# Kernel tuning notes

Hardware: AMD Instinct MI355X
Metric: run time of the kernel (lower is better)

Reference implementation:

```python
import jax, jax.numpy as jnp
import numpy as np

N = 50000      # nodes
E = 800000     # edges (before self-loops)
HEADS = 4
IN = 128
HID = 96
DH = HID // HEADS  # 24 per-head channels
G = 64         # graphs in batch
OUT = 3


def setup_inputs() -> dict:
    key = jax.random.key(0)
    ks = jax.random.split(key, 16)
    def w(k, shape, fan):
        return (jax.random.normal(k, shape, jnp.float32) * (fan ** -0.5)).astype(jnp.float32)
    x = jax.random.normal(ks[0], (N, IN), jnp.float32)
    edge_index = jax.random.randint(ks[1], (2, E), 0, N, dtype=jnp.int32)
    batch = jnp.sort(jax.random.randint(ks[2], (N,), 0, G, dtype=jnp.int32))
    return {
        'x': x, 'edge_index': edge_index, 'batch': batch, 'num_graphs': G,
        'W1': w(ks[3], (IN, HID), IN),
        'att_src1': w(ks[4], (HEADS, DH), DH),
        'att_dst1': w(ks[5], (HEADS, DH), DH),
        'b1': jnp.zeros((HID,), jnp.float32),
        'W2': w(ks[6], (HID, HID), HID),
        'att_src2': w(ks[7], (HEADS, DH), DH),
        'att_dst2': w(ks[8], (HEADS, DH), DH),
        'b2': jnp.zeros((HID,), jnp.float32),
        'g_w1': w(ks[9], (HID, HID // 2), HID),
        'g_b1': jnp.zeros((HID // 2,), jnp.float32),
        'g_w2': w(ks[10], (HID // 2, 1), HID // 2),
        'g_b2': jnp.zeros((1,), jnp.float32),
        'f_w1': w(ks[11], (HID, HID), HID),
        'f_b1': jnp.zeros((HID,), jnp.float32),
        'f_w2': w(ks[12], (HID, OUT), HID),
        'f_b2': jnp.zeros((OUT,), jnp.float32),
    }


def _gat_layer(x, src, dst, W, a_src, a_dst, b, n):
    # x: [n, F]; src/dst: [E'] (self-loops included). PyG GATConv math.
    h = (x @ W).reshape(n, HEADS, DH)                 # [n, H, d]
    alpha_s = jnp.sum(h * a_src[None], axis=-1)       # [n, H]
    alpha_d = jnp.sum(h * a_dst[None], axis=-1)       # [n, H]
    e = jax.nn.leaky_relu(alpha_s[src] + alpha_d[dst], 0.2)  # [E', H]
    # segment softmax over incoming edges of each dst node
    m = jax.ops.segment_max(e, dst, num_segments=n)   # [n, H]
    ex = jnp.exp(e - m[dst])
    denom = jax.ops.segment_sum(ex, dst, num_segments=n)
    alpha = ex / (denom[dst] + 1e-16)                 # [E', H]
    msg = h[src] * alpha[:, :, None]                  # [E', H, d]
    out = jax.ops.segment_sum(msg, dst, num_segments=n)
    return out.reshape(n, HEADS * DH) + b


def reference(x, edge_index, batch, num_graphs, W1, att_src1, att_dst1, b1,
              W2, att_src2, att_dst2, b2, g_w1, g_b1, g_w2, g_b2,
              f_w1, f_b1, f_w2, f_b2):
    n = x.shape[0]
    loops = jnp.arange(n, dtype=edge_index.dtype)
    src = jnp.concatenate([edge_index[0], loops])     # add self-loops (PyG default)
    dst = jnp.concatenate([edge_index[1], loops])
    h = jax.nn.elu(_gat_layer(x, src, dst, W1, att_src1, att_dst1, b1, n))
    h = jax.nn.elu(_gat_layer(h, src, dst, W2, att_src2, att_dst2, b2, n))
    # GlobalAttention pool: gate_nn -> softmax over batch segments -> weighted sum
    gate = (jax.nn.relu(h @ g_w1 + g_b1) @ g_w2 + g_b2)[:, 0]   # [n]
    gm = jax.ops.segment_max(gate, batch, num_segments=num_graphs)
    gm = jnp.where(jnp.isfinite(gm), gm, 0.0)
    ge = jnp.exp(gate - gm[batch])
    gden = jax.ops.segment_sum(ge, batch, num_segments=num_graphs)
    wgt = ge / (gden[batch] + 1e-16)                  # [n]
    pooled = jax.ops.segment_sum(h * wgt[:, None], batch, num_segments=num_graphs)  # [G, HID]
    return jax.nn.relu(pooled @ f_w1 + f_b1) @ f_w2 + f_b2   # [G, 3]
```

## Files before the change

### kernel.cpp

```cpp
#include <hip/hip_runtime.h>
#include <cmath>


__global__ void init_deg_kernel(int* __restrict__ deg, int n) {
    int i = blockIdx.x * blockDim.x + threadIdx.x;
    if (i < n) deg[i] = 1;
}

__global__ void hist_kernel(const int* __restrict__ dst, int* __restrict__ deg, int E) {
    int e = blockIdx.x * blockDim.x + threadIdx.x;
    if (e < E) atomicAdd(&deg[dst[e]], 1);
}

__global__ void scan_bsum_kernel(const int* __restrict__ deg, int* __restrict__ bsum, int n) {
    __shared__ int s[256];
    int t = threadIdx.x;
    int base = blockIdx.x * 1024;
    int sum = 0;
#pragma unroll
    for (int j = 0; j < 4; j++) {
        int i = base + j * 256 + t;
        if (i < n) sum += deg[i];
    }
    s[t] = sum;
    __syncthreads();
    for (int off = 128; off; off >>= 1) {
        if (t < off) s[t] += s[t + off];
        __syncthreads();
    }
    if (t == 0) bsum[blockIdx.x] = s[0];
}

__global__ void scan_bsum_scan_kernel(int* __restrict__ bsum, int nb,
                                      int* __restrict__ rowptr, int n) {
    __shared__ int s[256];
    int t = threadIdx.x;
    int v = (t < nb) ? bsum[t] : 0;
    s[t] = v;
    __syncthreads();
    for (int off = 1; off < 256; off <<= 1) {
        int x = (t >= off) ? s[t - off] : 0;
        __syncthreads();
        s[t] += x;
        __syncthreads();
    }
    if (t < nb) bsum[t] = s[t] - v;
    if (t == 255) rowptr[n] = s[255];
}

__global__ void scan_local_kernel(const int* __restrict__ deg, const int* __restrict__ bsum,
                                  int* __restrict__ rowptr, int* __restrict__ pos, int n) {
    __shared__ int s[256];
    int t = threadIdx.x;
    int base = blockIdx.x * 1024;
    int d[4];
    int sum = 0;
#pragma unroll
    for (int j = 0; j < 4; j++) {
        int i = base + t * 4 + j;
        d[j] = (i < n) ? deg[i] : 0;
        sum += d[j];
    }
    s[t] = sum;
    __syncthreads();
    for (int off = 1; off < 256; off <<= 1) {
        int x = (t >= off) ? s[t - off] : 0;
        __syncthreads();
        s[t] += x;
        __syncthreads();
    }
    int run = bsum[blockIdx.x] + s[t] - sum;
#pragma unroll
    for (int j = 0; j < 4; j++) {
        int i = base + t * 4 + j;
        if (i < n) { rowptr[i] = run; pos[i] = run; }
        run += d[j];
    }
}

__global__ void fill_kernel(const int* __restrict__ src, const int* __restrict__ dst,
                            int* __restrict__ pos, int* __restrict__ col, int E, int N) {
    int i = blockIdx.x * blockDim.x + threadIdx.x;
    if (i < E) {
        int p = atomicAdd(&pos[dst[i]], 1);
        col[p] = src[i];
    } else if (i < E + N) {
        int n = i - E;
        int p = atomicAdd(&pos[n], 1);
        col[p] = n;
    }
}

template<int K, int NCOL, int TN, int MODE>
__global__ __launch_bounds__(256)
void tiled_gemm_kernel(const float* __restrict__ X, const float* __restrict__ W,
                       const float* __restrict__ v1, const float* __restrict__ v2,
                       const float* __restrict__ v3,
                       float* __restrict__ H, float* __restrict__ AS, float* __restrict__ AD,
                       int n_nodes) {
    const int t = threadIdx.x;
    const int tx = t & 15, ty = t >> 4;
    const int c0 = tx * TN;
    const int m0 = ty * 4;
    const int node0 = blockIdx.x * 64;

    __shared__ float As[16][68];
    __shared__ float Bs[16][NCOL];

    float acc[4][TN];
#pragma unroll
    for (int i = 0; i < 4; i++)
#pragma unroll
        for (int j = 0; j < TN; j++) acc[i][j] = 0.f;

    const int am = t >> 2, akq = t & 3;

    for (int kb = 0; kb < K; kb += 16) {
        float4 av = make_float4(0.f, 0.f, 0.f, 0.f);
        int anode = node0 + am;
        if (anode < n_nodes)
            av = *reinterpret_cast<const float4*>(X + (size_t)anode * K + kb + akq * 4);
        As[akq * 4 + 0][am] = av.x;
        As[akq * 4 + 1][am] = av.y;
        As[akq * 4 + 2][am] = av.z;
        As[akq * 4 + 3][am] = av.w;
        {
            const float4* wsrc = reinterpret_cast<const float4*>(W + (size_t)kb * NCOL);
            float4* bdst = reinterpret_cast<float4*>(&Bs[0][0]);
            for (int i = t; i < 16 * NCOL / 4; i += 256) bdst[i] = wsrc[i];
        }
        __syncthreads();
#pragma unroll
        for (int k = 0; k < 16; k++) {
            float4 a4 = *reinterpret_cast<const float4*>(&As[k][m0]);
            float a[4] = {a4.x, a4.y, a4.z, a4.w};
            float b[TN];
            if constexpr ((TN & 1) == 0) {
#pragma unroll
                for (int j = 0; j < TN / 2; j++) {
                    float2 b2 = *reinterpret_cast<const float2*>(&Bs[k][c0 + 2 * j]);
                    b[2 * j] = b2.x; b[2 * j + 1] = b2.y;
                }
            } else {
#pragma unroll
                for (int j = 0; j < TN; j++) b[j] = Bs[k][c0 + j];
            }
#pragma unroll
            for (int i = 0; i < 4; i++)
#pragma unroll
                for (int j = 0; j < TN; j++)
                    acc[i][j] = fmaf(a[i], b[j], acc[i][j]);
        }
        __syncthreads();
    }

    if constexpr (MODE == 0) {
        __shared__ float s_as[64][16];
        __shared__ float s_ad[64][16];
#pragma unroll
        for (int i = 0; i < 4; i++) {
            int node = node0 + m0 + i;
            float asp = 0.f, adp = 0.f;
#pragma unroll
            for (int j = 0; j < TN; j++) {
                asp = fmaf(acc[i][j], v1[c0 + j], asp);
                adp = fmaf(acc[i][j], v2[c0 + j], adp);
            }
            s_as[m0 + i][tx] = asp;
            s_ad[m0 + i][tx] = adp;
            if (node < n_nodes) {
#pragma unroll
                for (int j = 0; j < TN / 2; j++) {
                    float2 o;
                    o.x = acc[i][2 * j]; o.y = acc[i][2 * j + 1];
                    *reinterpret_cast<float2*>(H + (size_t)node * NCOL + c0 + 2 * j) = o;
                }
            }
        }
        __syncthreads();
        int m = t >> 2, head = t & 3;
        int node = node0 + m;
        if (node < n_nodes) {
            float s1 = s_as[m][head * 4 + 0] + s_as[m][head * 4 + 1]
                     + s_as[m][head * 4 + 2] + s_as[m][head * 4 + 3];
            float s2 = s_ad[m][head * 4 + 0] + s_ad[m][head * 4 + 1]
                     + s_ad[m][head * 4 + 2] + s_ad[m][head * 4 + 3];
            AS[(size_t)node * 4 + head] = s1;
            AD[(size_t)node * 4 + head] = s2;
        }
    } else {
        __shared__ float s_g[64][16];
#pragma unroll
        for (int i = 0; i < 4; i++) {
            float p = 0.f;
#pragma unroll
            for (int j = 0; j < TN; j++) {
                float a = acc[i][j] + v1[c0 + j];
                a = fmaxf(a, 0.f);
                p = fmaf(a, v2[c0 + j], p);
            }
            s_g[m0 + i][tx] = p;
        }
        __syncthreads();
        if (t < 64) {
            int node = node0 + t;
            if (node < n_nodes) {
                float s = 0.f;
#pragma unroll
                for (int j = 0; j < 16; j++) s += s_g[t][j];
                H[node] = s + v3[0];
            }
        }
    }
}

__global__ __launch_bounds__(256)
void gat_agg_wave_kernel(const float* __restrict__ H, const float* __restrict__ AS,
                         const float* __restrict__ AD, const int* __restrict__ rowptr,
                         const int* __restrict__ col, const float* __restrict__ bias,
                         float* __restrict__ OUT, int n_nodes) {
    int wid = threadIdx.x >> 6;
    int lane = threadIdx.x & 63;
    int n = blockIdx.x * 4 + wid;
    if (n >= n_nodes) return;
    int beg = rowptr[n];
    int deg = rowptr[n + 1] - beg;

    int h = lane & 3;
    int slot = lane >> 2;
    float ad_n = AD[(size_t)n * 4 + h];

    float mymax = -INFINITY;
    for (int i = slot; i < deg; i += 16) {
        int s = col[beg + i];
        float v = AS[(size_t)s * 4 + h] + ad_n;
        v = v > 0.f ? v : 0.2f * v;
        mymax = fmaxf(mymax, v);
    }
#pragma unroll
    for (int m = 4; m <= 32; m <<= 1)
        mymax = fmaxf(mymax, __shfl_xor(mymax, m, 64));
    float m_h = mymax;

    int c = lane;
    bool cown = c < 48;
    int head_c = cown ? (c / 12) : 0;
    const float2* __restrict__ Hc = reinterpret_cast<const float2*>(H) + c;

    float denom_part = 0.f;
    float2 acc0 = make_float2(0.f, 0.f), acc1 = make_float2(0.f, 0.f);
    float2 acc2 = make_float2(0.f, 0.f), acc3 = make_float2(0.f, 0.f);

    for (int base = 0; base < deg; base += 16) {
        int ce = base + slot;
        int s_e = 0;
        float ex = 0.f;
        if (ce < deg) {
            s_e = col[beg + ce];
            float v = AS[(size_t)s_e * 4 + h] + ad_n;
            v = v > 0.f ? v : 0.2f * v;
            ex = __expf(v - m_h);
        }
        denom_part += ex;
        int cnt = min(16, deg - base);

        int sbv[16];
        float wv[16];
#pragma unroll
        for (int i = 0; i < 16; i++) {
            sbv[i] = __shfl(s_e, i * 4, 64);
            wv[i]  = __shfl(ex,  i * 4 + head_c, 64);
        }

#pragma unroll
        for (int g = 0; g < 16; g += 4) {
            if (g < cnt && cown) {
                float2 v0 = Hc[(size_t)sbv[g + 0] * 48];
                float2 v1 = Hc[(size_t)sbv[g + 1] * 48];
                float2 v2 = Hc[(size_t)sbv[g + 2] * 48];
                float2 v3 = Hc[(size_t)sbv[g + 3] * 48];
                acc0.x = fmaf(v0.x, wv[g + 0], acc0.x);
                acc0.y = fmaf(v0.y, wv[g + 0], acc0.y);
                acc1.x = fmaf(v1.x, wv[g + 1], acc1.x);
                acc1.y = fmaf(v1.y, wv[g + 1], acc1.y);
                acc2.x = fmaf(v2.x, wv[g + 2], acc2.x);
                acc2.y = fmaf(v2.y, wv[g + 2], acc2.y);
                acc3.x = fmaf(v3.x, wv[g + 3], acc3.x);
                acc3.y = fmaf(v3.y, wv[g + 3], acc3.y);
            }
        }
    }

#pragma unroll
    for (int m = 4; m <= 32; m <<= 1)
        denom_part += __shfl_xor(denom_part, m, 64);
    float den = __shfl(denom_part, head_c, 64);

    if (cown) {
        float2 acc;
        acc.x = (acc0.x + acc1.x) + (acc2.x + acc3.x);
        acc.y = (acc0.y + acc1.y) + (acc2.y + acc3.y);
        float2 b2 = reinterpret_cast<const float2*>(bias)[c];
        float inv = 1.f / (den + 1e-16f);
        float ox = acc.x * inv + b2.x;
        float oy = acc.y * inv + b2.y;
        ox = ox > 0.f ? ox : (__expf(ox) - 1.f);
        oy = oy > 0.f ? oy : (__expf(oy) - 1.f);
        reinterpret_cast<float2*>(OUT)[(size_t)n * 48 + c] = make_float2(ox, oy);
    }
}

__device__ __forceinline__ int lower_bound_dev(const int* __restrict__ arr, int n, int key) {
    int lo = 0, hi = n;
    while (lo < hi) {
        int mid = (lo + hi) >> 1;
        if (arr[mid] < key) lo = mid + 1; else hi = mid;
    }
    return lo;
}

__global__ void gate_stats_kernel(const float* __restrict__ gate, const int* __restrict__ batch,
                                  int n_nodes, float* __restrict__ gm_out,
                                  float* __restrict__ inv_gden_out, float* __restrict__ pooled) {
    int g = blockIdx.x, t = threadIdx.x;
    if (t < 96) pooled[(size_t)g * 96 + t] = 0.f;
    __shared__ int sb, se;
    __shared__ float sred[256];
    if (t == 0) {
        sb = lower_bound_dev(batch, n_nodes, g);
        se = lower_bound_dev(batch, n_nodes, g + 1);
    }
    __syncthreads();
    int beg = sb, end = se;

    float mx = -INFINITY;
    for (int i = beg + t; i < end; i += 256) mx = fmaxf(mx, gate[i]);
    sred[t] = mx;
    __syncthreads();
    for (int off = 128; off; off >>= 1) {
        if (t < off) sred[t] = fmaxf(sred[t], sred[t + off]);
        __syncthreads();
    }
    float gm = sred[0];
    if (!isfinite(gm)) gm = 0.f;
    __syncthreads();

    float sm = 0.f;
    for (int i = beg + t; i < end; i += 256) sm += __expf(gate[i] - gm);
    sred[t] = sm;
    __syncthreads();
    for (int off = 128; off; off >>= 1) {
        if (t < off) sred[t] += sred[t + off];
        __syncthreads();
    }
    if (t == 0) {
        gm_out[g] = gm;
        inv_gden_out[g] = 1.f / (sred[0] + 1e-16f);
    }
}

__global__ __launch_bounds__(384)
void pool_accum_kernel(const float* __restrict__ H2, const float* __restrict__ gate,
                       const int* __restrict__ batch, const float* __restrict__ gm,
                       const float* __restrict__ inv_gden, int n_nodes,
                       float* __restrict__ pooled) {
    const int NPB = 256;
    int t = threadIdx.x;
    int group = t / 96;
    int c = t - group * 96;
    if (group >= 4) return;
    int nbeg = blockIdx.x * NPB;
    int nend = min(nbeg + NPB, n_nodes);

    float acc = 0.f;
    int curg = -1;
    for (int i = nbeg + group; i < nend; i += 4) {
        int g = batch[i];
        if (g != curg) {
            if (curg >= 0) atomicAdd(&pooled[(size_t)curg * 96 + c], acc);
            acc = 0.f;
            curg = g;
        }
        float w = __expf(gate[i] - gm[curg]) * inv_gden[curg];
        acc = fmaf(w, H2[(size_t)i * 96 + c], acc);
    }
    if (curg >= 0) atomicAdd(&pooled[(size_t)curg * 96 + c], acc);
}

__global__ void final_kernel(const float* __restrict__ pooled, const float* __restrict__ f_w1,
                             const float* __restrict__ f_b1, const float* __restrict__ f_w2,
                             const float* __restrict__ f_b2, float* __restrict__ out) {
    int g = blockIdx.x, t = threadIdx.x;
    __shared__ float sp[96], sh[96];
    sp[t] = pooled[(size_t)g * 96 + t];
    __syncthreads();
    float a = f_b1[t];
    for (int k = 0; k < 96; k++) a = fmaf(sp[k], f_w1[k * 96 + t], a);
    sh[t] = fmaxf(a, 0.f);
    __syncthreads();
    if (t < 3) {
        float o = f_b2[t];
        for (int k = 0; k < 96; k++) o = fmaf(sh[k], f_w2[k * 3 + t], o);
        out[g * 3 + t] = o;
    }
}

extern "C" void kernel_launch(void* const* d_in, const int* in_sizes, int n_in,
                              void* d_out, int out_size, void* d_ws, size_t ws_size,
                              hipStream_t stream) {
    const float* x    = (const float*)d_in[0];
    const int*   ei   = (const int*)d_in[1];
    const int*   batch= (const int*)d_in[2];
    const float* W1   = (const float*)d_in[4];
    const float* as1  = (const float*)d_in[5];
    const float* ad1  = (const float*)d_in[6];
    const float* b1   = (const float*)d_in[7];
    const float* W2   = (const float*)d_in[8];
    const float* as2  = (const float*)d_in[9];
    const float* ad2  = (const float*)d_in[10];
    const float* b2   = (const float*)d_in[11];
    const float* g_w1 = (const float*)d_in[12];
    const float* g_b1 = (const float*)d_in[13];
    const float* g_w2 = (const float*)d_in[14];
    const float* g_b2 = (const float*)d_in[15];
    const float* f_w1 = (const float*)d_in[16];
    const float* f_b1 = (const float*)d_in[17];
    const float* f_w2 = (const float*)d_in[18];
    const float* f_b2 = (const float*)d_in[19];
    float* out = (float*)d_out;

    int N = in_sizes[0] / 128;
    int E = in_sizes[1] / 2;
    int G = out_size / 3;
    const int* srcv = ei;
    const int* dstv = ei + E;

    char* p = (char*)d_ws;
    auto alloc = [&](size_t bytes) {
        char* q = p;
        p += (bytes + 255) & ~(size_t)255;
        return q;
    };
    float* hA    = (float*)alloc((size_t)N * 96 * 4);
    float* hB    = (float*)alloc((size_t)N * 96 * 4);
    float* AS    = (float*)alloc((size_t)N * 4 * 4);
    float* AD    = (float*)alloc((size_t)N * 4 * 4);
    float* gatev = (float*)alloc((size_t)N * 4);
    float* pooled= (float*)alloc((size_t)G * 96 * 4);
    float* gmv   = (float*)alloc((size_t)G * 4);
    float* invgd = (float*)alloc((size_t)G * 4);
    int*   deg   = (int*)alloc((size_t)N * 4);
    int*   pos   = (int*)alloc((size_t)N * 4);
    int*   rowptr= (int*)alloc(((size_t)N + 1) * 4);
    int*   bsum  = (int*)alloc((size_t)256 * 4);
    int*   col   = (int*)alloc((size_t)(E + N) * 4);

    const int B = 256;
    int gemm_blocks = (N + 63) / 64;
    int nb_scan = (N + 1023) / 1024;

    init_deg_kernel<<<(N + B - 1) / B, B, 0, stream>>>(deg, N);
    hist_kernel<<<(E + B - 1) / B, B, 0, stream>>>(dstv, deg, E);
    scan_bsum_kernel<<<nb_scan, 256, 0, stream>>>(deg, bsum, N);
    scan_bsum_scan_kernel<<<1, 256, 0, stream>>>(bsum, nb_scan, rowptr, N);
    scan_local_kernel<<<nb_scan, 256, 0, stream>>>(deg, bsum, rowptr, pos, N);
    fill_kernel<<<(E + N + B - 1) / B, B, 0, stream>>>(srcv, dstv, pos, col, E, N);

    tiled_gemm_kernel<128, 96, 6, 0><<<gemm_blocks, 256, 0, stream>>>(
        x, W1, as1, ad1, nullptr, hA, AS, AD, N);
    gat_agg_wave_kernel<<<(N + 3) / 4, 256, 0, stream>>>(hA, AS, AD, rowptr, col, b1, hB, N);
    tiled_gemm_kernel<96, 96, 6, 0><<<gemm_blocks, 256, 0, stream>>>(
        hB, W2, as2, ad2, nullptr, hA, AS, AD, N);
    gat_agg_wave_kernel<<<(N + 3) / 4, 256, 0, stream>>>(hA, AS, AD, rowptr, col, b2, hB, N);

    tiled_gemm_kernel<96, 48, 3, 1><<<gemm_blocks, 256, 0, stream>>>(
        hB, g_w1, g_b1, g_w2, g_b2, gatev, nullptr, nullptr, N);
    gate_stats_kernel<<<G, 256, 0, stream>>>(gatev, batch, N, gmv, invgd, pooled);
    pool_accum_kernel<<<(N + 255) / 256, 384, 0, stream>>>(
        hB, gatev, batch, gmv, invgd, N, pooled);
    final_kernel<<<G, 96, 0, stream>>>(pooled, f_w1, f_b1, f_w2, f_b2, out);
}
```

Measured before the change: 352.4 us.

## Drop softmax max passes, fuse GEMM with degree histogram, merge scan kernels

Removes the max-subtraction pass in both GAT edge softmaxes and in the pooling softmax. Edge weights become exp(e) directly, and the pooling denominator is accumulated by atomics alongside the weighted sums and normalised in the final kernel. The first GEMM and the degree histogram now run as one launch, the three scan kernels shrink to two, one memset replaces the init kernels, and the gather inner loop is unrolled to 8 loads. This cuts a full edge pass per layer and several launches, at the cost of possible exp overflow when logits are large.

```diff
diff --git a/kernel.cpp b/kernel.cpp
--- a/kernel.cpp
+++ b/kernel.cpp
@@ -1,108 +1,19 @@
 #include <hip/hip_runtime.h>
 #include <cmath>
 
-
-__global__ void init_deg_kernel(int* __restrict__ deg, int n) {
-    int i = blockIdx.x * blockDim.x + threadIdx.x;
-    if (i < n) deg[i] = 1;
-}
-
-__global__ void hist_kernel(const int* __restrict__ dst, int* __restrict__ deg, int E) {
-    int e = blockIdx.x * blockDim.x + threadIdx.x;
-    if (e < E) atomicAdd(&deg[dst[e]], 1);
-}
-
-__global__ void scan_bsum_kernel(const int* __restrict__ deg, int* __restrict__ bsum, int n) {
-    __shared__ int s[256];
-    int t = threadIdx.x;
-    int base = blockIdx.x * 1024;
-    int sum = 0;
-#pragma unroll
-    for (int j = 0; j < 4; j++) {
-        int i = base + j * 256 + t;
-        if (i < n) sum += deg[i];
-    }
-    s[t] = sum;
-    __syncthreads();
-    for (int off = 128; off; off >>= 1) {
-        if (t < off) s[t] += s[t + off];
-        __syncthreads();
-    }
-    if (t == 0) bsum[blockIdx.x] = s[0];
-}
-
-__global__ void scan_bsum_scan_kernel(int* __restrict__ bsum, int nb,
-                                      int* __restrict__ rowptr, int n) {
-    __shared__ int s[256];
-    int t = threadIdx.x;
-    int v = (t < nb) ? bsum[t] : 0;
-    s[t] = v;
-    __syncthreads();
-    for (int off = 1; off < 256; off <<= 1) {
-        int x = (t >= off) ? s[t - off] : 0;
-        __syncthreads();
-        s[t] += x;
-        __syncthreads();
-    }
-    if (t < nb) bsum[t] = s[t] - v;
-    if (t == 255) rowptr[n] = s[255];
-}
-
-__global__ void scan_local_kernel(const int* __restrict__ deg, const int* __restrict__ bsum,
-                                  int* __restrict__ rowptr, int* __restrict__ pos, int n) {
-    __shared__ int s[256];
-    int t = threadIdx.x;
-    int base = blockIdx.x * 1024;
-    int d[4];
-    int sum = 0;
-#pragma unroll
-    for (int j = 0; j < 4; j++) {
-        int i = base + t * 4 + j;
-        d[j] = (i < n) ? deg[i] : 0;
-        sum += d[j];
-    }
-    s[t] = sum;
-    __syncthreads();
-    for (int off = 1; off < 256; off <<= 1) {
-        int x = (t >= off) ? s[t - off] : 0;
-        __syncthreads();
-        s[t] += x;
-        __syncthreads();
-    }
-    int run = bsum[blockIdx.x] + s[t] - sum;
-#pragma unroll
-    for (int j = 0; j < 4; j++) {
-        int i = base + t * 4 + j;
-        if (i < n) { rowptr[i] = run; pos[i] = run; }
-        run += d[j];
-    }
-}
-
-__global__ void fill_kernel(const int* __restrict__ src, const int* __restrict__ dst,
-                            int* __restrict__ pos, int* __restrict__ col, int E, int N) {
-    int i = blockIdx.x * blockDim.x + threadIdx.x;
-    if (i < E) {
-        int p = atomicAdd(&pos[dst[i]], 1);
-        col[p] = src[i];
-    } else if (i < E + N) {
-        int n = i - E;
-        int p = atomicAdd(&pos[n], 1);
-        col[p] = n;
-    }
-}
-
 template<int K, int NCOL, int TN, int MODE>
-__global__ __launch_bounds__(256)
-void tiled_gemm_kernel(const float* __restrict__ X, const float* __restrict__ W,
-                       const float* __restrict__ v1, const float* __restrict__ v2,
-                       const float* __restrict__ v3,
-                       float* __restrict__ H, float* __restrict__ AS, float* __restrict__ AD,
-                       int n_nodes) {
+__device__ __forceinline__ void gemm_body(int bid, const float* __restrict__ X,
+                                          const float* __restrict__ W,
+                                          const float* __restrict__ v1,
+                                          const float* __restrict__ v2,
+                                          const float* __restrict__ v3,
+                                          float* __restrict__ H, float* __restrict__ AS,
+                                          float* __restrict__ AD, int n_nodes) {
     const int t = threadIdx.x;
     const int tx = t & 15, ty = t >> 4;
     const int c0 = tx * TN;
     const int m0 = ty * 4;
-    const int node0 = blockIdx.x * 64;
+    const int node0 = bid * 64;
 
     __shared__ float As[16][68];
     __shared__ float Bs[16][NCOL];
@@ -214,55 +125,142 @@
     }
 }
 
+template<int K, int NCOL, int TN, int MODE>
 __global__ __launch_bounds__(256)
-void gat_agg_wave_kernel(const float* __restrict__ H, const float* __restrict__ AS,
-                         const float* __restrict__ AD, const int* __restrict__ rowptr,
-                         const int* __restrict__ col, const float* __restrict__ bias,
-                         float* __restrict__ OUT, int n_nodes) {
-    int wid = threadIdx.x >> 6;
-    int lane = threadIdx.x & 63;
+void tiled_gemm_kernel(const float* __restrict__ X, const float* __restrict__ W,
+                       const float* __restrict__ v1, const float* __restrict__ v2,
+                       const float* __restrict__ v3,
+                       float* __restrict__ H, float* __restrict__ AS, float* __restrict__ AD,
+                       int n_nodes) {
+    gemm_body<K, NCOL, TN, MODE>(blockIdx.x, X, W, v1, v2, v3, H, AS, AD, n_nodes);
+}
+
+template<int K, int NCOL, int TN>
+__global__ __launch_bounds__(256)
+void gemm_hist_kernel(const float* __restrict__ X, const float* __restrict__ W,
+                      const float* __restrict__ v1, const float* __restrict__ v2,
+                      float* __restrict__ H, float* __restrict__ AS, float* __restrict__ AD,
+                      int n_nodes, int nb_gemm,
+                      const int* __restrict__ dst, int* __restrict__ deg, int E) {
+    if ((int)blockIdx.x < nb_gemm) {
+        gemm_body<K, NCOL, TN, 0>(blockIdx.x, X, W, v1, v2, nullptr, H, AS, AD, n_nodes);
+    } else {
+        int tid = (blockIdx.x - nb_gemm) * 256 + threadIdx.x;
+        int stride = (gridDim.x - nb_gemm) * 256;
+        for (int e = tid; e < E; e += stride) atomicAdd(&deg[dst[e]], 1);
+    }
+}
+
+__global__ void scan_bsum_kernel(const int* __restrict__ deg, int* __restrict__ bsum, int n) {
+    __shared__ int s[256];
+    int t = threadIdx.x;
+    int base = blockIdx.x * 1024;
+    int sum = 0;
+#pragma unroll
+    for (int j = 0; j < 4; j++) {
+        int i = base + j * 256 + t;
+        if (i < n) sum += deg[i] + 1;
+    }
+    s[t] = sum;
+    __syncthreads();
+    for (int off = 128; off; off >>= 1) {
+        if (t < off) s[t] += s[t + off];
+        __syncthreads();
+    }
+    if (t == 0) bsum[blockIdx.x] = s[0];
+}
+
+__global__ void scan_local_kernel(const int* __restrict__ deg, const int* __restrict__ bsum,
+                                  int nb, int* __restrict__ rowptr, int* __restrict__ pos,
+                                  int n) {
+    __shared__ int s[256];
+    __shared__ int boff[257];
+    int t = threadIdx.x;
+    if (t < nb) boff[t] = bsum[t];
+    __syncthreads();
+    if (t == 0) {
+        int run = 0;
+        for (int i = 0; i < nb; i++) { int v = boff[i]; boff[i] = run; run += v; }
+        boff[nb] = run;
+    }
+    __syncthreads();
+    if (blockIdx.x == 0 && t == 0) rowptr[n] = boff[nb];
+
+    int base = blockIdx.x * 1024;
+    int d[4];
+    int sum = 0;
+#pragma unroll
+    for (int j = 0; j < 4; j++) {
+        int i = base + t * 4 + j;
+        d[j] = (i < n) ? deg[i] + 1 : 0;
+        sum += d[j];
+    }
+    s[t] = sum;
+    __syncthreads();
+    for (int off = 1; off < 256; off <<= 1) {
+        int x = (t >= off) ? s[t - off] : 0;
+        __syncthreads();
+        s[t] += x;
+        __syncthreads();
+    }
+    int run = boff[blockIdx.x] + s[t] - sum;
+#pragma unroll
+    for (int j = 0; j < 4; j++) {
+        int i = base + t * 4 + j;
+        if (i < n) { rowptr[i] = run; pos[i] = run; }
+        run += d[j];
+    }
+}
+
+__global__ void fill_kernel(const int* __restrict__ src, const int* __restrict__ dst,
+                            int* __restrict__ pos, int* __restrict__ col, int E, int N) {
+    int i = blockIdx.x * blockDim.x + threadIdx.x;
+    if (i < E) {
+        int p = atomicAdd(&pos[dst[i]], 1);
+        col[p] = src[i];
+    } else if (i < E + N) {
+        int n = i - E;
+        int p = atomicAdd(&pos[n], 1);
+        col[p] = n;
+    }
+}
+
+__global__ __launch_bounds__(256)
+void gat_gather_kernel(const float* __restrict__ H, const float* __restrict__ AS,
+                       const float* __restrict__ AD, const int* __restrict__ rowptr,
+                       const int* __restrict__ col, const float* __restrict__ bias,
+                       float* __restrict__ OUT, int n_nodes) {
+    int wid = threadIdx.x >> 6, lane = threadIdx.x & 63;
     int n = blockIdx.x * 4 + wid;
     if (n >= n_nodes) return;
-    int beg = rowptr[n];
-    int deg = rowptr[n + 1] - beg;
-
-    int h = lane & 3;
-    int slot = lane >> 2;
+    int beg = rowptr[n], end = rowptr[n + 1];
+
+    int h = lane & 3, slot = lane >> 2;
     float ad_n = AD[(size_t)n * 4 + h];
-
-    float mymax = -INFINITY;
-    for (int i = slot; i < deg; i += 16) {
-        int s = col[beg + i];
-        float v = AS[(size_t)s * 4 + h] + ad_n;
-        v = v > 0.f ? v : 0.2f * v;
-        mymax = fmaxf(mymax, v);
-    }
-#pragma unroll
-    for (int m = 4; m <= 32; m <<= 1)
-        mymax = fmaxf(mymax, __shfl_xor(mymax, m, 64));
-    float m_h = mymax;
 
     int c = lane;
     bool cown = c < 48;
     int head_c = cown ? (c / 12) : 0;
     const float2* __restrict__ Hc = reinterpret_cast<const float2*>(H) + c;
 
-    float denom_part = 0.f;
+    float denom = 0.f;
     float2 acc0 = make_float2(0.f, 0.f), acc1 = make_float2(0.f, 0.f);
     float2 acc2 = make_float2(0.f, 0.f), acc3 = make_float2(0.f, 0.f);
-
-    for (int base = 0; base < deg; base += 16) {
+    float2 acc4 = make_float2(0.f, 0.f), acc5 = make_float2(0.f, 0.f);
+    float2 acc6 = make_float2(0.f, 0.f), acc7 = make_float2(0.f, 0.f);
+
+    for (int base = beg; base < end; base += 16) {
         int ce = base + slot;
         int s_e = 0;
         float ex = 0.f;
-        if (ce < deg) {
-            s_e = col[beg + ce];
+        if (ce < end) {
+            s_e = col[ce];
             float v = AS[(size_t)s_e * 4 + h] + ad_n;
             v = v > 0.f ? v : 0.2f * v;
-            ex = __expf(v - m_h);
-        }
-        denom_part += ex;
-        int cnt = min(16, deg - base);
+            ex = __expf(v);
+        }
+        denom += ex;
+        int cnt = end - base;
 
         int sbv[16];
         float wv[16];
@@ -273,97 +271,51 @@
         }
 
 #pragma unroll
-        for (int g = 0; g < 16; g += 4) {
+        for (int g = 0; g < 16; g += 8) {
             if (g < cnt && cown) {
                 float2 v0 = Hc[(size_t)sbv[g + 0] * 48];
                 float2 v1 = Hc[(size_t)sbv[g + 1] * 48];
                 float2 v2 = Hc[(size_t)sbv[g + 2] * 48];
                 float2 v3 = Hc[(size_t)sbv[g + 3] * 48];
-                acc0.x = fmaf(v0.x, wv[g + 0], acc0.x);
-                acc0.y = fmaf(v0.y, wv[g + 0], acc0.y);
-                acc1.x = fmaf(v1.x, wv[g + 1], acc1.x);
-                acc1.y = fmaf(v1.y, wv[g + 1], acc1.y);
-                acc2.x = fmaf(v2.x, wv[g + 2], acc2.x);
-                acc2.y = fmaf(v2.y, wv[g + 2], acc2.y);
-                acc3.x = fmaf(v3.x, wv[g + 3], acc3.x);
-                acc3.y = fmaf(v3.y, wv[g + 3], acc3.y);
+                float2 v4 = Hc[(size_t)sbv[g + 4] * 48];
+                float2 v5 = Hc[(size_t)sbv[g + 5] * 48];
+                float2 v6 = Hc[(size_t)sbv[g + 6] * 48];
+                float2 v7 = Hc[(size_t)sbv[g + 7] * 48];
+                acc0.x = fmaf(v0.x, wv[g + 0], acc0.x); acc0.y = fmaf(v0.y, wv[g + 0], acc0.y);
+                acc1.x = fmaf(v1.x, wv[g + 1], acc1.x); acc1.y = fmaf(v1.y, wv[g + 1], acc1.y);
+                acc2.x = fmaf(v2.x, wv[g + 2], acc2.x); acc2.y = fmaf(v2.y, wv[g + 2], acc2.y);
+                acc3.x = fmaf(v3.x, wv[g + 3], acc3.x); acc3.y = fmaf(v3.y, wv[g + 3], acc3.y);
+                acc4.x = fmaf(v4.x, wv[g + 4], acc4.x); acc4.y = fmaf(v4.y, wv[g + 4], acc4.y);
+                acc5.x = fmaf(v5.x, wv[g + 5], acc5.x); acc5.y = fmaf(v5.y, wv[g + 5], acc5.y);
+                acc6.x = fmaf(v6.x, wv[g + 6], acc6.x); acc6.y = fmaf(v6.y, wv[g + 6], acc6.y);
+                acc7.x = fmaf(v7.x, wv[g + 7], acc7.x); acc7.y = fmaf(v7.y, wv[g + 7], acc7.y);
             }
         }
     }
 
 #pragma unroll
     for (int m = 4; m <= 32; m <<= 1)
-        denom_part += __shfl_xor(denom_part, m, 64);
-    float den = __shfl(denom_part, head_c, 64);
+        denom += __shfl_xor(denom, m, 64);
+    float den = __shfl(denom, head_c, 64);
 
     if (cown) {
-        float2 acc;
-        acc.x = (acc0.x + acc1.x) + (acc2.x + acc3.x);
-        acc.y = (acc0.y + acc1.y) + (acc2.y + acc3.y);
+        float2 a;
+        a.x = ((acc0.x + acc1.x) + (acc2.x + acc3.x)) + ((acc4.x + acc5.x) + (acc6.x + acc7.x));
+        a.y = ((acc0.y + acc1.y) + (acc2.y + acc3.y)) + ((acc4.y + acc5.y) + (acc6.y + acc7.y));
         float2 b2 = reinterpret_cast<const float2*>(bias)[c];
         float inv = 1.f / (den + 1e-16f);
-        float ox = acc.x * inv + b2.x;
-        float oy = acc.y * inv + b2.y;
+        float ox = a.x * inv + b2.x;
+        float oy = a.y * inv + b2.y;
         ox = ox > 0.f ? ox : (__expf(ox) - 1.f);
         oy = oy > 0.f ? oy : (__expf(oy) - 1.f);
         reinterpret_cast<float2*>(OUT)[(size_t)n * 48 + c] = make_float2(ox, oy);
     }
 }
 
-__device__ __forceinline__ int lower_bound_dev(const int* __restrict__ arr, int n, int key) {
-    int lo = 0, hi = n;
-    while (lo < hi) {
-        int mid = (lo + hi) >> 1;
-        if (arr[mid] < key) lo = mid + 1; else hi = mid;
-    }
-    return lo;
-}
-
-__global__ void gate_stats_kernel(const float* __restrict__ gate, const int* __restrict__ batch,
-                                  int n_nodes, float* __restrict__ gm_out,
-                                  float* __restrict__ inv_gden_out, float* __restrict__ pooled) {
-    int g = blockIdx.x, t = threadIdx.x;
-    if (t < 96) pooled[(size_t)g * 96 + t] = 0.f;
-    __shared__ int sb, se;
-    __shared__ float sred[256];
-    if (t == 0) {
-        sb = lower_bound_dev(batch, n_nodes, g);
-        se = lower_bound_dev(batch, n_nodes, g + 1);
-    }
-    __syncthreads();
-    int beg = sb, end = se;
-
-    float mx = -INFINITY;
-    for (int i = beg + t; i < end; i += 256) mx = fmaxf(mx, gate[i]);
-    sred[t] = mx;
-    __syncthreads();
-    for (int off = 128; off; off >>= 1) {
-        if (t < off) sred[t] = fmaxf(sred[t], sred[t + off]);
-        __syncthreads();
-    }
-    float gm = sred[0];
-    if (!isfinite(gm)) gm = 0.f;
-    __syncthreads();
-
-    float sm = 0.f;
-    for (int i = beg + t; i < end; i += 256) sm += __expf(gate[i] - gm);
-    sred[t] = sm;
-    __syncthreads();
-    for (int off = 128; off; off >>= 1) {
-        if (t < off) sred[t] += sred[t + off];
-        __syncthreads();
-    }
-    if (t == 0) {
-        gm_out[g] = gm;
-        inv_gden_out[g] = 1.f / (sred[0] + 1e-16f);
-    }
-}
-
 __global__ __launch_bounds__(384)
 void pool_accum_kernel(const float* __restrict__ H2, const float* __restrict__ gate,
-                       const int* __restrict__ batch, const float* __restrict__ gm,
-                       const float* __restrict__ inv_gden, int n_nodes,
-                       float* __restrict__ pooled) {
+                       const int* __restrict__ batch, int n_nodes,
+                       float* __restrict__ pooled, float* __restrict__ denp) {
     const int NPB = 256;
     int t = threadIdx.x;
     int group = t / 96;
@@ -372,27 +324,35 @@
     int nbeg = blockIdx.x * NPB;
     int nend = min(nbeg + NPB, n_nodes);
 
-    float acc = 0.f;
+    float acc = 0.f, dacc = 0.f;
     int curg = -1;
     for (int i = nbeg + group; i < nend; i += 4) {
         int g = batch[i];
         if (g != curg) {
-            if (curg >= 0) atomicAdd(&pooled[(size_t)curg * 96 + c], acc);
-            acc = 0.f;
+            if (curg >= 0) {
+                atomicAdd(&pooled[(size_t)curg * 96 + c], acc);
+                if (c == 0) atomicAdd(&denp[curg], dacc);
+            }
+            acc = 0.f; dacc = 0.f;
             curg = g;
         }
-        float w = __expf(gate[i] - gm[curg]) * inv_gden[curg];
-        acc = fmaf(w, H2[(size_t)i * 96 + c], acc);
-    }
-    if (curg >= 0) atomicAdd(&pooled[(size_t)curg * 96 + c], acc);
-}
-
-__global__ void final_kernel(const float* __restrict__ pooled, const float* __restrict__ f_w1,
-                             const float* __restrict__ f_b1, const float* __restrict__ f_w2,
-                             const float* __restrict__ f_b2, float* __restrict__ out) {
+        float ge = __expf(gate[i]);
+        acc = fmaf(ge, H2[(size_t)i * 96 + c], acc);
+        if (c == 0) dacc += ge;
+    }
+    if (curg >= 0) {
+        atomicAdd(&pooled[(size_t)curg * 96 + c], acc);
+        if (c == 0) atomicAdd(&denp[curg], dacc);
+    }
+}
+
+__global__ void final_kernel(const float* __restrict__ pooled, const float* __restrict__ denp,
+                             const float* __restrict__ f_w1, const float* __restrict__ f_b1,
+                             const float* __restrict__ f_w2, const float* __restrict__ f_b2,
+                             float* __restrict__ out) {
     int g = blockIdx.x, t = threadIdx.x;
     __shared__ float sp[96], sh[96];
-    sp[t] = pooled[(size_t)g * 96 + t];
+    sp[t] = pooled[(size_t)g * 96 + t] / (denp[g] + 1e-16f);
     __syncthreads();
     float a = f_b1[t];
     for (int k = 0; k < 96; k++) a = fmaf(sp[k], f_w1[k * 96 + t], a);
@@ -435,7 +395,13 @@
     const int* srcv = ei;
     const int* dstv = ei + E;
 
-    char* p = (char*)d_ws;
+    char* base = (char*)d_ws;
+    int*   deg    = (int*)base;
+    float* pooled = (float*)(base + (size_t)N * 4);
+    float* denp   = (float*)(base + (size_t)N * 4 + (size_t)G * 96 * 4);
+    size_t zbytes = (size_t)(N + G * 96 + G) * 4;
+
+    char* p = base + ((zbytes + 255) & ~(size_t)255);
     auto alloc = [&](size_t bytes) {
         char* q = p;
         p += (bytes + 255) & ~(size_t)255;
@@ -446,10 +412,6 @@
     float* AS    = (float*)alloc((size_t)N * 4 * 4);
     float* AD    = (float*)alloc((size_t)N * 4 * 4);
     float* gatev = (float*)alloc((size_t)N * 4);
-    float* pooled= (float*)alloc((size_t)G * 96 * 4);
-    float* gmv   = (float*)alloc((size_t)G * 4);
-    float* invgd = (float*)alloc((size_t)G * 4);
-    int*   deg   = (int*)alloc((size_t)N * 4);
     int*   pos   = (int*)alloc((size_t)N * 4);
     int*   rowptr= (int*)alloc(((size_t)N + 1) * 4);
     int*   bsum  = (int*)alloc((size_t)256 * 4);
@@ -459,24 +421,23 @@
     int gemm_blocks = (N + 63) / 64;
     int nb_scan = (N + 1023) / 1024;
 
-    init_deg_kernel<<<(N + B - 1) / B, B, 0, stream>>>(deg, N);
-    hist_kernel<<<(E + B - 1) / B, B, 0, stream>>>(dstv, deg, E);
+    hipMemsetAsync(base, 0, zbytes, stream);
+
+    gemm_hist_kernel<128, 96, 6><<<gemm_blocks + 256, 256, 0, stream>>>(
+        x, W1, as1, ad1, hA, AS, AD, N, gemm_blocks, dstv, deg, E);
+
     scan_bsum_kernel<<<nb_scan, 256, 0, stream>>>(deg, bsum, N);
-    scan_bsum_scan_kernel<<<1, 256, 0, stream>>>(bsum, nb_scan, rowptr, N);
-    scan_local_kernel<<<nb_scan, 256, 0, stream>>>(deg, bsum, rowptr, pos, N);
+    scan_local_kernel<<<nb_scan, 256, 0, stream>>>(deg, bsum, nb_scan, rowptr, pos, N);
     fill_kernel<<<(E + N + B - 1) / B, B, 0, stream>>>(srcv, dstv, pos, col, E, N);
 
-    tiled_gemm_kernel<128, 96, 6, 0><<<gemm_blocks, 256, 0, stream>>>(
-        x, W1, as1, ad1, nullptr, hA, AS, AD, N);
-    gat_agg_wave_kernel<<<(N + 3) / 4, 256, 0, stream>>>(hA, AS, AD, rowptr, col, b1, hB, N);
+    gat_gather_kernel<<<(N + 3) / 4, 256, 0, stream>>>(hA, AS, AD, rowptr, col, b1, hB, N);
     tiled_gemm_kernel<96, 96, 6, 0><<<gemm_blocks, 256, 0, stream>>>(
         hB, W2, as2, ad2, nullptr, hA, AS, AD, N);
-    gat_agg_wave_kernel<<<(N + 3) / 4, 256, 0, stream>>>(hA, AS, AD, rowptr, col, b2, hB, N);
+    gat_gather_kernel<<<(N + 3) / 4, 256, 0, stream>>>(hA, AS, AD, rowptr, col, b2, hB, N);
 
     tiled_gemm_kernel<96, 48, 3, 1><<<gemm_blocks, 256, 0, stream>>>(
         hB, g_w1, g_b1, g_w2, g_b2, gatev, nullptr, nullptr, N);
-    gate_stats_kernel<<<G, 256, 0, stream>>>(gatev, batch, N, gmv, invgd, pooled);
     pool_accum_kernel<<<(N + 255) / 256, 384, 0, stream>>>(
-        hB, gatev, batch, gmv, invgd, N, pooled);
-    final_kernel<<<G, 96, 0, stream>>>(pooled, f_w1, f_b1, f_w2, f_b2, out);
-}
+        hB, gatev, batch, N, pooled, denp);
+    final_kernel<<<G, 96, 0, stream>>>(pooled, denp, f_w1, f_b1, f_w2, f_b2, out);
+}
```

Result: faster. 322.3 us (-8.5%).
